# Performance work log

Measured on AMD Instinct MI355X. Metric: run time of the kernel, lower is better.

The kernel has to match this reference:

```python
import jax, jax.numpy as jnp
import numpy as np

N_NODES = 100000
N_EDGES = 3200000
N_GRAPHS = 512
F_IN, F_HID, F_OUT = 64, 16, 2


def gcn_conv(x, W, b, row, col, ew, n_nodes):
    # PyG GCNConv (normalize=True, add_self_loops=True, fill_value=1.0):
    # out = D^{-1/2} (A + I) D^{-1/2} X W + b, edge weights included.
    loop = jnp.arange(n_nodes, dtype=row.dtype)
    row_f = jnp.concatenate([row, loop])
    col_f = jnp.concatenate([col, loop])
    ew_f = jnp.concatenate([ew, jnp.ones((n_nodes,), dtype=ew.dtype)])
    deg = jax.ops.segment_sum(ew_f, col_f, num_segments=n_nodes)
    dinv = jnp.where(deg > 0, jax.lax.rsqrt(jnp.where(deg > 0, deg, 1.0)), 0.0)
    norm = dinv[row_f] * ew_f * dinv[col_f]          # [E+N]
    h = x @ W                                        # [N, F_out] dense GEMM first (cheaper gather)
    msg = norm[:, None] * h[row_f]                   # gather + scale
    out = jax.ops.segment_sum(msg, col_f, num_segments=n_nodes)  # scatter-add
    return out + b


def setup_inputs() -> dict:
    key = jax.random.key(0)
    ks = jax.random.split(key, 10)
    x = jax.random.normal(ks[0], (N_NODES, F_IN), dtype=jnp.float32)
    edge_index = jax.random.randint(ks[1], (2, N_EDGES), 0, N_NODES, dtype=jnp.int64)
    edge_weight = jax.random.uniform(ks[2], (N_EDGES,), dtype=jnp.float32)
    batch = jnp.sort(jax.random.randint(ks[3], (N_NODES,), 0, N_GRAPHS, dtype=jnp.int64))
    s1 = 1.0 / np.sqrt(F_IN)
    s2 = 1.0 / np.sqrt(F_HID)
    W1 = jax.random.uniform(ks[4], (F_IN, F_HID), minval=-s1, maxval=s1, dtype=jnp.float32)
    b1 = jnp.zeros((F_HID,), dtype=jnp.float32)
    W2 = jax.random.uniform(ks[5], (F_HID, F_HID), minval=-s2, maxval=s2, dtype=jnp.float32)
    b2 = jnp.zeros((F_HID,), dtype=jnp.float32)
    Wfc = jax.random.uniform(ks[6], (F_HID, F_OUT), minval=-s2, maxval=s2, dtype=jnp.float32)
    bfc = jax.random.uniform(ks[7], (F_OUT,), minval=-s2, maxval=s2, dtype=jnp.float32)
    return {"x": x, "edge_index": edge_index, "edge_weight": edge_weight, "batch": batch,
            "W1": W1, "b1": b1, "W2": W2, "b2": b2, "Wfc": Wfc, "bfc": bfc}


def reference(x, edge_index, edge_weight, batch, W1, b1, W2, b2, Wfc, bfc):
    row, col = edge_index[0], edge_index[1]
    n = x.shape[0]
    h = gcn_conv(x, W1, b1, row, col, edge_weight, n)
    h = jax.nn.relu(h)
    # dropout p=0.2 is identity in eval mode
    h = gcn_conv(h, W2, b2, row, col, edge_weight, n)
    h = jax.nn.relu(h)
    # global_mean_pool over graph ids
    sums = jax.ops.segment_sum(h, batch, num_segments=N_GRAPHS)
    counts = jax.ops.segment_sum(jnp.ones((n,), dtype=h.dtype), batch, num_segments=N_GRAPHS)
    pooled = sums / jnp.maximum(counts, 1.0)[:, None]
    logits = pooled @ Wfc + bfc
    return jax.nn.log_softmax(logits, axis=1)
```

## Files before the change

### kernel.cpp

```cpp
#include <hip/hip_runtime.h>


#define BSH   6
#define BN    64
#define NB    1563
#define BCAP  2432
#define BCAP2 2688
#define CHUNK 8192
#define DEQ   (1.0f / 511.0f)

__device__ __forceinline__ float bf2f(unsigned short u) {
    return __uint_as_float(((unsigned)u) << 16);
}
__device__ __forceinline__ unsigned short f2bf(float f) {
    unsigned b = __float_as_uint(f);
    return (unsigned short)((b + 0x7FFFu + ((b >> 16) & 1u)) >> 16);
}

__global__ void bin_kernel(const int* __restrict__ row, const int* __restrict__ col,
                           const float* __restrict__ ew, unsigned* __restrict__ gcur,
                           unsigned* __restrict__ recs, int E) {
    __shared__ unsigned lcnt[NB];
    __shared__ unsigned lbase[NB];
    int tid = threadIdx.x;
    int e0 = blockIdx.x * CHUNK;
    int e1 = e0 + CHUNK; if (e1 > E) e1 = E;
    for (int i = tid; i < NB; i += blockDim.x) lcnt[i] = 0;
    __syncthreads();
    for (int e = e0 + tid; e < e1; e += blockDim.x)
        atomicAdd(&lcnt[((unsigned)col[e]) >> BSH], 1u);
    __syncthreads();
    for (int i = tid; i < NB; i += blockDim.x) lbase[i] = atomicAdd(&gcur[i], lcnt[i]);
    __syncthreads();
    for (int i = tid; i < NB; i += blockDim.x) lcnt[i] = 0;
    __syncthreads();
    for (int e = e0 + tid; e < e1; e += blockDim.x) {
        unsigned c = (unsigned)col[e];
        unsigned b = c >> BSH;
        unsigned q = __float2uint_rn(ew[e] * 511.0f);
        unsigned r = atomicAdd(&lcnt[b], 1u);
        unsigned slot = lbase[b] + r;
        if (slot < BCAP)
            recs[(size_t)b * BCAP + slot] = ((c & (BN - 1u)) << 26)
                                          | ((unsigned)row[e] << 9) | q;
    }
}

__global__ void __launch_bounds__(256) csr_kernel(
        const unsigned* __restrict__ recs, const unsigned* __restrict__ gcur,
        float* __restrict__ dinv, unsigned* __restrict__ s_off,
        unsigned* __restrict__ ecnt, unsigned* __restrict__ epack, int N) {
    __shared__ unsigned combo[BN];
    __shared__ unsigned pre[BN];
    __shared__ unsigned cur[BN];
    __shared__ unsigned stot;
    __shared__ unsigned srt[BCAP2];
    int b = blockIdx.x, tid = threadIdx.x;
    if (tid < BN) { combo[tid] = 0; cur[tid] = 0; }
    for (int k = tid; k < BCAP2; k += 256) srt[k] = 0;
    __syncthreads();
    int n = (int)gcur[b]; if (n > BCAP) n = BCAP;
    const unsigned* rb = recs + (size_t)b * BCAP;
    for (int k = tid; k < n; k += 256) {
        unsigned r = rb[k];
        atomicAdd(&combo[r >> 26], (1u << 20) | (r & 511u));
    }
    __syncthreads();
    if (tid < 64) {
        unsigned cb  = combo[tid];
        unsigned cnt = cb >> 20;
        float    deg = (float)(cb & 0xFFFFFu) * DEQ;
        unsigned asz = (cnt + 3u) & ~3u;
        unsigned sc = asz;
#pragma unroll
        for (int d = 1; d < 64; d <<= 1) {
            unsigned t2 = __shfl_up(sc, d, 64);
            if (tid >= d) sc += t2;
        }
        unsigned base = sc - asz;
        pre[tid] = base;
        if (tid == 63) stot = sc;
        int i = (b << BSH) + tid;
        if (i < N) {
            dinv[i]  = rsqrtf(deg + 1.0f);
            s_off[i] = (unsigned)b * BCAP2 + base;
            ecnt[i]  = asz;
        }
    }
    __syncthreads();
    for (int k = tid; k < n; k += 256) {
        unsigned r = rb[k];
        unsigned o = r >> 26;
        unsigned p = pre[o] + atomicAdd(&cur[o], 1u);
        if (p < (unsigned)BCAP2) srt[p] = r & 0x03FFFFFFu;
    }
    __syncthreads();
    unsigned tot = stot; if (tot > (unsigned)BCAP2) tot = BCAP2;
    unsigned* eb = epack + (size_t)b * BCAP2;
    for (unsigned k = tid; k < tot; k += 256) eb[k] = srt[k];
}

__global__ void bounds_kernel(const int* __restrict__ batch, unsigned* __restrict__ gfirst,
                              unsigned* __restrict__ gend, int N) {
    int i = blockIdx.x * blockDim.x + threadIdx.x;
    if (i >= N) return;
    int g = batch[i];
    if (i == 0 || batch[i - 1] != g) gfirst[g] = (unsigned)i;
    if (i == N - 1 || batch[i + 1] != g) gend[g] = (unsigned)(i + 1);
}

__global__ void gemm1_kernel(const float* __restrict__ x, const float* __restrict__ W1,
                             const float* __restrict__ dinv, unsigned short* __restrict__ ys,
                             int N) {
    __shared__ float Ws[64 * 16];
    for (int k = threadIdx.x; k < 64 * 16; k += blockDim.x) Ws[k] = W1[k];
    __syncthreads();
    int i = blockIdx.x * blockDim.x + threadIdx.x;
    if (i >= N) return;
    const float4* xp = reinterpret_cast<const float4*>(x + (size_t)i * 64);
    float acc[16];
#pragma unroll
    for (int j = 0; j < 16; ++j) acc[j] = 0.0f;
#pragma unroll
    for (int k4 = 0; k4 < 16; ++k4) {
        float4 xv = xp[k4];
#pragma unroll
        for (int j = 0; j < 16; ++j) {
            acc[j] += xv.x * Ws[(k4 * 4 + 0) * 16 + j]
                    + xv.y * Ws[(k4 * 4 + 1) * 16 + j]
                    + xv.z * Ws[(k4 * 4 + 2) * 16 + j]
                    + xv.w * Ws[(k4 * 4 + 3) * 16 + j];
        }
    }
    float d = dinv[i];
    unsigned pk[8];
#pragma unroll
    for (int q = 0; q < 8; ++q)
        pk[q] = (unsigned)f2bf(d * acc[2 * q]) | ((unsigned)f2bf(d * acc[2 * q + 1]) << 16);
    uint4* op = reinterpret_cast<uint4*>(ys + (size_t)i * 16);
    op[0] = make_uint4(pk[0], pk[1], pk[2], pk[3]);
    op[1] = make_uint4(pk[4], pk[5], pk[6], pk[7]);
}

#define GREC(r, accq) { unsigned _r = (r); \
    accq += (float)(_r & 511u) * bf2f(ys[(size_t)(_r >> 9) * 16 + j]); }

__global__ void gconv1_kernel(const unsigned* __restrict__ s_off, const unsigned* __restrict__ ecnt,
                              const unsigned* __restrict__ epack, const float* __restrict__ dinv,
                              const unsigned short* __restrict__ ys,
                              const float* __restrict__ b1, const float* __restrict__ W2,
                              unsigned short* __restrict__ ys2, int N) {
    __shared__ float Ws[16 * 16];
    __shared__ float bs[16];
    if (threadIdx.x < 16 * 16) Ws[threadIdx.x] = W2[threadIdx.x];
    if (threadIdx.x < 16) bs[threadIdx.x] = b1[threadIdx.x];
    __syncthreads();
    int t = blockIdx.x * blockDim.x + threadIdx.x;
    int i = t >> 4, j = t & 15;
    if (i >= N) return;
    unsigned s = s_off[i], m = ecnt[i];
    const uint4* ep4 = reinterpret_cast<const uint4*>(epack + s);
    float accq = 0.0f;
    unsigned q4 = m >> 2, k = 0;
    for (; k + 2 <= q4; k += 2) {
        uint4 a = ep4[k], b4 = ep4[k + 1];
        GREC(a.x, accq); GREC(a.y, accq); GREC(a.z, accq); GREC(a.w, accq);
        GREC(b4.x, accq); GREC(b4.y, accq); GREC(b4.z, accq); GREC(b4.w, accq);
    }
    if (k < q4) {
        uint4 a = ep4[k];
        GREC(a.x, accq); GREC(a.y, accq); GREC(a.z, accq); GREC(a.w, accq);
    }
    float acc = bf2f(ys[(size_t)i * 16 + j]) + accq * DEQ;
    float d = dinv[i];
    float h = fmaxf(d * acc + bs[j], 0.0f);
    float acc2 = 0.0f;
#pragma unroll
    for (int kk = 0; kk < 16; ++kk) {
        float hk = __shfl(h, kk, 16);
        acc2 += hk * Ws[kk * 16 + j];
    }
    ys2[(size_t)i * 16 + j] = f2bf(d * acc2);
}

__global__ void gconv2_kernel(const unsigned* __restrict__ s_off, const unsigned* __restrict__ ecnt,
                              const unsigned* __restrict__ epack, const float* __restrict__ dinv,
                              const unsigned short* __restrict__ ys,
                              const float* __restrict__ bias, float* __restrict__ hbuf, int N) {
    int t = blockIdx.x * blockDim.x + threadIdx.x;
    int i = t >> 4, j = t & 15;
    if (i >= N) return;
    unsigned s = s_off[i], m = ecnt[i];
    const uint4* ep4 = reinterpret_cast<const uint4*>(epack + s);
    float accq = 0.0f;
    unsigned q4 = m >> 2, k = 0;
    for (; k + 2 <= q4; k += 2) {
        uint4 a = ep4[k], b4 = ep4[k + 1];
        GREC(a.x, accq); GREC(a.y, accq); GREC(a.z, accq); GREC(a.w, accq);
        GREC(b4.x, accq); GREC(b4.y, accq); GREC(b4.z, accq); GREC(b4.w, accq);
    }
    if (k < q4) {
        uint4 a = ep4[k];
        GREC(a.x, accq); GREC(a.y, accq); GREC(a.z, accq); GREC(a.w, accq);
    }
    float acc = bf2f(ys[(size_t)i * 16 + j]) + accq * DEQ;
    hbuf[(size_t)i * 16 + j] = fmaxf(dinv[i] * acc + bias[j], 0.0f);
}

__global__ void pool_kernel(const float* __restrict__ hbuf, const unsigned* __restrict__ gfirst,
                            const unsigned* __restrict__ gend, float* __restrict__ pooled, int G) {
    __shared__ float part[16][16];
    int g = blockIdx.x;
    unsigned s = gfirst[g], e = (s == 0xFFFFFFFFu) ? 0u : gend[g];
    int tid = threadIdx.x;
    int grp = tid >> 4, j = tid & 15;
    float acc = 0.0f;
    if (s != 0xFFFFFFFFu)
        for (unsigned i = s + grp; i < e; i += 16)
            acc += hbuf[(size_t)i * 16 + j];
    part[grp][j] = acc;
    __syncthreads();
    if (grp == 0) {
        float sum = 0.0f;
#pragma unroll
        for (int k = 0; k < 16; ++k) sum += part[k][j];
        float cnt = (s == 0xFFFFFFFFu) ? 1.0f : fmaxf((float)(e - s), 1.0f);
        pooled[g * 16 + j] = sum / cnt;
    }
}

__global__ void head_kernel(const float* __restrict__ pooled, const float* __restrict__ Wfc,
                            const float* __restrict__ bfc, float* __restrict__ out, int G) {
    int g = blockIdx.x * blockDim.x + threadIdx.x;
    if (g >= G) return;
    float l0 = bfc[0], l1 = bfc[1];
#pragma unroll
    for (int j = 0; j < 16; ++j) {
        float p = pooled[g * 16 + j];
        l0 += p * Wfc[j * 2 + 0];
        l1 += p * Wfc[j * 2 + 1];
    }
    float m = fmaxf(l0, l1);
    float lse = m + logf(expf(l0 - m) + expf(l1 - m));
    out[g * 2 + 0] = l0 - lse;
    out[g * 2 + 1] = l1 - lse;
}

__global__ void deg_at_kernel(const int* __restrict__ col, const float* __restrict__ ew,
                              float* __restrict__ deg, int E) {
    int t = blockIdx.x * blockDim.x + threadIdx.x;
    if (t < E) atomicAdd(&deg[col[t]], ew[t]);
}
__global__ void dinv_at_kernel(float* __restrict__ deg, const int* __restrict__ batch,
                               float* __restrict__ cntg, int N) {
    int i = blockIdx.x * blockDim.x + threadIdx.x;
    if (i >= N) return;
    deg[i] = rsqrtf(deg[i] + 1.0f);
    atomicAdd(&cntg[batch[i]], 1.0f);
}
__global__ void selfloop_kernel(const float* __restrict__ xw, const float* __restrict__ dinv,
                                float* __restrict__ out, int N) {
    int t = blockIdx.x * blockDim.x + threadIdx.x;
    if (t >= N * 16) return;
    float d = dinv[t >> 4];
    out[t] = d * d * xw[t];
}
__global__ void edge_at_kernel(const int* __restrict__ row, const int* __restrict__ col,
                               const float* __restrict__ ew, const float* __restrict__ dinv,
                               const float* __restrict__ xw, float* __restrict__ out, int E) {
    int t = blockIdx.x * blockDim.x + threadIdx.x;
    if (t >= E * 16) return;
    int e = t >> 4, j = t & 15;
    int r = row[e], c = col[e];
    float norm = dinv[r] * ew[e] * dinv[c];
    atomicAdd(&out[c * 16 + j], norm * xw[r * 16 + j]);
}
__global__ void pool_at_kernel(const float* __restrict__ h, const float* __restrict__ b2,
                               const int* __restrict__ batch, float* __restrict__ pooled, int N) {
    int t = blockIdx.x * blockDim.x + threadIdx.x;
    if (t >= N * 16) return;
    int i = t >> 4, j = t & 15;
    float v = fmaxf(h[t] + b2[j], 0.0f);
    atomicAdd(&pooled[batch[i] * 16 + j], v);
}
__global__ void head_at_kernel(const float* __restrict__ pooled, const float* __restrict__ cntg,
                               const float* __restrict__ Wfc, const float* __restrict__ bfc,
                               float* __restrict__ out, int G) {
    int g = blockIdx.x * blockDim.x + threadIdx.x;
    if (g >= G) return;
    float c = fmaxf(cntg[g], 1.0f);
    float l0 = bfc[0], l1 = bfc[1];
#pragma unroll
    for (int j = 0; j < 16; ++j) {
        float p = pooled[g * 16 + j] / c;
        l0 += p * Wfc[j * 2 + 0];
        l1 += p * Wfc[j * 2 + 1];
    }
    float m = fmaxf(l0, l1);
    float lse = m + logf(expf(l0 - m) + expf(l1 - m));
    out[g * 2 + 0] = l0 - lse;
    out[g * 2 + 1] = l1 - lse;
}
__global__ void gemm1p_kernel(const float* __restrict__ x, const float* __restrict__ W1,
                              float* __restrict__ xw, int N) {
    __shared__ float Ws[64 * 16];
    for (int k = threadIdx.x; k < 64 * 16; k += blockDim.x) Ws[k] = W1[k];
    __syncthreads();
    int i = blockIdx.x * blockDim.x + threadIdx.x;
    if (i >= N) return;
    const float4* xp = reinterpret_cast<const float4*>(x + (size_t)i * 64);
    float acc[16];
#pragma unroll
    for (int j = 0; j < 16; ++j) acc[j] = 0.0f;
#pragma unroll
    for (int k4 = 0; k4 < 16; ++k4) {
        float4 xv = xp[k4];
#pragma unroll
        for (int j = 0; j < 16; ++j) {
            acc[j] += xv.x * Ws[(k4 * 4 + 0) * 16 + j]
                    + xv.y * Ws[(k4 * 4 + 1) * 16 + j]
                    + xv.z * Ws[(k4 * 4 + 2) * 16 + j]
                    + xv.w * Ws[(k4 * 4 + 3) * 16 + j];
        }
    }
    float4* op = reinterpret_cast<float4*>(xw + (size_t)i * 16);
    op[0] = make_float4(acc[0],acc[1],acc[2],acc[3]);
    op[1] = make_float4(acc[4],acc[5],acc[6],acc[7]);
    op[2] = make_float4(acc[8],acc[9],acc[10],acc[11]);
    op[3] = make_float4(acc[12],acc[13],acc[14],acc[15]);
}
__global__ void gemm2p_kernel(const float* __restrict__ in, const float* __restrict__ b,
                              const float* __restrict__ W, float* __restrict__ xw, int N) {
    __shared__ float Ws[16 * 16];
    __shared__ float bs[16];
    if (threadIdx.x < 16 * 16) Ws[threadIdx.x] = W[threadIdx.x];
    if (threadIdx.x < 16) bs[threadIdx.x] = b[threadIdx.x];
    __syncthreads();
    int i = blockIdx.x * blockDim.x + threadIdx.x;
    if (i >= N) return;
    const float4* ip = reinterpret_cast<const float4*>(in + (size_t)i * 16);
    float h[16];
#pragma unroll
    for (int q = 0; q < 4; ++q) {
        float4 v = ip[q];
        h[q*4+0] = fmaxf(v.x + bs[q*4+0], 0.0f);
        h[q*4+1] = fmaxf(v.y + bs[q*4+1], 0.0f);
        h[q*4+2] = fmaxf(v.z + bs[q*4+2], 0.0f);
        h[q*4+3] = fmaxf(v.w + bs[q*4+3], 0.0f);
    }
    float acc[16];
#pragma unroll
    for (int j = 0; j < 16; ++j) acc[j] = 0.0f;
#pragma unroll
    for (int k = 0; k < 16; ++k)
#pragma unroll
        for (int j = 0; j < 16; ++j) acc[j] += h[k] * Ws[k * 16 + j];
    float4* op = reinterpret_cast<float4*>(xw + (size_t)i * 16);
    op[0] = make_float4(acc[0],acc[1],acc[2],acc[3]);
    op[1] = make_float4(acc[4],acc[5],acc[6],acc[7]);
    op[2] = make_float4(acc[8],acc[9],acc[10],acc[11]);
    op[3] = make_float4(acc[12],acc[13],acc[14],acc[15]);
}

extern "C" void kernel_launch(void* const* d_in, const int* in_sizes, int n_in,
                              void* d_out, int out_size, void* d_ws, size_t ws_size,
                              hipStream_t stream) {
    const float* x   = (const float*)d_in[0];
    const int*   ei  = (const int*)d_in[1];
    const float* ew  = (const float*)d_in[2];
    const int*   bat = (const int*)d_in[3];
    const float* W1  = (const float*)d_in[4];
    const float* b1  = (const float*)d_in[5];
    const float* W2  = (const float*)d_in[6];
    const float* b2  = (const float*)d_in[7];
    const float* Wfc = (const float*)d_in[8];
    const float* bfc = (const float*)d_in[9];
    float* out = (float*)d_out;

    const int N = in_sizes[0] / 64;
    const int E = in_sizes[2];
    const int G = out_size / 2;

    const int* row = ei;
    const int* col = ei + E;
    const size_t n16 = (size_t)N * 16;
    const int nb = (N + BN - 1) >> BSH;

    const size_t need = (size_t)NB * BCAP * 4
                      + (size_t)NB * BCAP2 * 4
                      + n16 * 2 * 2
                      + n16 * 4
                      + ((size_t)N * 3 + NB + (size_t)G * 18) * 4;

    const int B = 256;
    const int nbN   = (N + B - 1) / B;
    const int nbN16 = (int)((n16 + B - 1) / B);

    if (ws_size >= need && nb <= NB) {
        unsigned*       recs  = (unsigned*)d_ws;
        unsigned*       epack = recs + (size_t)NB * BCAP;
        unsigned short* ys    = (unsigned short*)(epack + (size_t)NB * BCAP2);
        unsigned short* ys2   = ys + n16;
        float*          hbuf  = (float*)(ys2 + n16);
        float*          dinv  = hbuf + n16;
        unsigned*       s_off = (unsigned*)(dinv + N);
        unsigned*       ecnt  = s_off + N;
        unsigned*       gcur  = ecnt + N;
        unsigned*       gfirst= gcur + NB;
        unsigned*       gend  = gfirst + G;
        float*          pooled= (float*)(gend + G);

        hipMemsetAsync(gcur, 0, (size_t)NB * 4, stream);
        hipMemsetAsync(gfirst, 0xFF, (size_t)G * 4, stream);
        hipMemsetAsync(gend, 0, (size_t)G * 4, stream);

        const int nbBin = (E + CHUNK - 1) / CHUNK;
        bin_kernel<<<nbBin, B, 0, stream>>>(row, col, ew, gcur, recs, E);
        csr_kernel<<<nb, B, 0, stream>>>(recs, gcur, dinv, s_off, ecnt, epack, N);
        bounds_kernel<<<nbN, B, 0, stream>>>(bat, gfirst, gend, N);

        gemm1_kernel<<<nbN, B, 0, stream>>>(x, W1, dinv, ys, N);
        gconv1_kernel<<<nbN16, B, 0, stream>>>(s_off, ecnt, epack, dinv, ys, b1, W2, ys2, N);
        gconv2_kernel<<<nbN16, B, 0, stream>>>(s_off, ecnt, epack, dinv, ys2, b2, hbuf, N);
        pool_kernel<<<G, B, 0, stream>>>(hbuf, gfirst, gend, pooled, G);
        head_kernel<<<(G + B - 1) / B, B, 0, stream>>>(pooled, Wfc, bfc, out, G);
    } else {
        float* xw1    = (float*)d_ws;
        float* out1   = xw1 + n16;
        float* dinv   = out1 + n16;
        float* pooled = dinv + N;
        float* cntg   = pooled + (size_t)G * 16;

        hipMemsetAsync(dinv, 0, (size_t)(N + G * 16 + G) * 4, stream);

        const int nbE   = (E + B - 1) / B;
        const int nbE16 = (int)(((long long)E * 16 + B - 1) / B);
        deg_at_kernel<<<nbE, B, 0, stream>>>(col, ew, dinv, E);
        dinv_at_kernel<<<nbN, B, 0, stream>>>(dinv, bat, cntg, N);
        gemm1p_kernel<<<nbN, B, 0, stream>>>(x, W1, xw1, N);
        selfloop_kernel<<<nbN16, B, 0, stream>>>(xw1, dinv, out1, N);
        edge_at_kernel<<<nbE16, B, 0, stream>>>(row, col, ew, dinv, xw1, out1, E);
        gemm2p_kernel<<<nbN, B, 0, stream>>>(out1, b1, W2, xw1, N);
        selfloop_kernel<<<nbN16, B, 0, stream>>>(xw1, dinv, out1, N);
        edge_at_kernel<<<nbE16, B, 0, stream>>>(row, col, ew, dinv, xw1, out1, E);
        pool_at_kernel<<<nbN16, B, 0, stream>>>(out1, b2, bat, pooled, N);
        head_at_kernel<<<(G + B - 1) / B, B, 0, stream>>>(pooled, cntg, Wfc, bfc, out, G);
    }
}
```

Before: 236.3 us.

## Partition edge-binning buffers per XCD to localize global atomics and writes

The bin kernel now reads the hardware XCC id and uses a separate counter array and record buffer for each of the 8 XCDs, so the global atomics on bin cursors and the scattered record writes stay within one XCD's L2. The CSR kernel then walks all 8 partitions per bin to build the degree sums and the sorted edge lists. The aim is to cut cross-die coherence traffic and atomic contention on the shared counters. In exchange it adds more workspace, 8 reads per bin in the CSR pass, and a per-partition capacity (RCAP) that could overflow if one XCD's share of a bin is skewed.

```diff
diff --git a/kernel.cpp b/kernel.cpp
--- a/kernel.cpp
+++ b/kernel.cpp
@@ -4,6 +4,8 @@
 #define BSH   6
 #define BN    64
 #define NB    1563
+#define NXCD  8
+#define RCAP  448
 #define BCAP  2432
 #define BCAP2 2688
 #define CHUNK 8192
@@ -16,13 +18,19 @@
     unsigned b = __float_as_uint(f);
     return (unsigned short)((b + 0x7FFFu + ((b >> 16) & 1u)) >> 16);
 }
+__device__ __forceinline__ int get_xcc() {
+    int x;
+    asm volatile("s_getreg_b32 %0, hwreg(HW_REG_XCC_ID)" : "=s"(x));
+    return x & (NXCD - 1);
+}
 
 __global__ void bin_kernel(const int* __restrict__ row, const int* __restrict__ col,
-                           const float* __restrict__ ew, unsigned* __restrict__ gcur,
-                           unsigned* __restrict__ recs, int E) {
+                           const float* __restrict__ ew, unsigned* __restrict__ gcur8,
+                           unsigned* __restrict__ recs8, int E) {
     __shared__ unsigned lcnt[NB];
     __shared__ unsigned lbase[NB];
     int tid = threadIdx.x;
+    int xcc = get_xcc();
     int e0 = blockIdx.x * CHUNK;
     int e1 = e0 + CHUNK; if (e1 > E) e1 = E;
     for (int i = tid; i < NB; i += blockDim.x) lcnt[i] = 0;
@@ -30,24 +38,26 @@
     for (int e = e0 + tid; e < e1; e += blockDim.x)
         atomicAdd(&lcnt[((unsigned)col[e]) >> BSH], 1u);
     __syncthreads();
-    for (int i = tid; i < NB; i += blockDim.x) lbase[i] = atomicAdd(&gcur[i], lcnt[i]);
+    unsigned* gc = gcur8 + (size_t)xcc * NB;
+    for (int i = tid; i < NB; i += blockDim.x) lbase[i] = atomicAdd(&gc[i], lcnt[i]);
     __syncthreads();
     for (int i = tid; i < NB; i += blockDim.x) lcnt[i] = 0;
     __syncthreads();
+    unsigned* rr = recs8 + (size_t)xcc * NB * RCAP;
     for (int e = e0 + tid; e < e1; e += blockDim.x) {
         unsigned c = (unsigned)col[e];
         unsigned b = c >> BSH;
         unsigned q = __float2uint_rn(ew[e] * 511.0f);
         unsigned r = atomicAdd(&lcnt[b], 1u);
         unsigned slot = lbase[b] + r;
-        if (slot < BCAP)
-            recs[(size_t)b * BCAP + slot] = ((c & (BN - 1u)) << 26)
-                                          | ((unsigned)row[e] << 9) | q;
+        if (slot < RCAP)
+            rr[(size_t)b * RCAP + slot] = ((c & (BN - 1u)) << 26)
+                                        | ((unsigned)row[e] << 9) | q;
     }
 }
 
 __global__ void __launch_bounds__(256) csr_kernel(
-        const unsigned* __restrict__ recs, const unsigned* __restrict__ gcur,
+        const unsigned* __restrict__ recs8, const unsigned* __restrict__ gcur8,
         float* __restrict__ dinv, unsigned* __restrict__ s_off,
         unsigned* __restrict__ ecnt, unsigned* __restrict__ epack, int N) {
     __shared__ unsigned combo[BN];
@@ -59,11 +69,13 @@
     if (tid < BN) { combo[tid] = 0; cur[tid] = 0; }
     for (int k = tid; k < BCAP2; k += 256) srt[k] = 0;
     __syncthreads();
-    int n = (int)gcur[b]; if (n > BCAP) n = BCAP;
-    const unsigned* rb = recs + (size_t)b * BCAP;
-    for (int k = tid; k < n; k += 256) {
-        unsigned r = rb[k];
-        atomicAdd(&combo[r >> 26], (1u << 20) | (r & 511u));
+    for (int x = 0; x < NXCD; ++x) {
+        int n = (int)gcur8[(size_t)x * NB + b]; if (n > RCAP) n = RCAP;
+        const unsigned* rb = recs8 + ((size_t)x * NB + b) * RCAP;
+        for (int k = tid; k < n; k += 256) {
+            unsigned r = rb[k];
+            atomicAdd(&combo[r >> 26], (1u << 20) | (r & 511u));
+        }
     }
     __syncthreads();
     if (tid < 64) {
@@ -88,11 +100,15 @@
         }
     }
     __syncthreads();
-    for (int k = tid; k < n; k += 256) {
-        unsigned r = rb[k];
-        unsigned o = r >> 26;
-        unsigned p = pre[o] + atomicAdd(&cur[o], 1u);
-        if (p < (unsigned)BCAP2) srt[p] = r & 0x03FFFFFFu;
+    for (int x = 0; x < NXCD; ++x) {
+        int n = (int)gcur8[(size_t)x * NB + b]; if (n > RCAP) n = RCAP;
+        const unsigned* rb = recs8 + ((size_t)x * NB + b) * RCAP;
+        for (int k = tid; k < n; k += 256) {
+            unsigned r = rb[k];
+            unsigned o = r >> 26;
+            unsigned p = pre[o] + atomicAdd(&cur[o], 1u);
+            if (p < (unsigned)BCAP2) srt[p] = r & 0x03FFFFFFu;
+        }
     }
     __syncthreads();
     unsigned tot = stot; if (tot > (unsigned)BCAP2) tot = BCAP2;
@@ -386,37 +402,37 @@
     const size_t n16 = (size_t)N * 16;
     const int nb = (N + BN - 1) >> BSH;
 
-    const size_t need = (size_t)NB * BCAP * 4
+    const size_t need = (size_t)NXCD * NB * RCAP * 4
                       + (size_t)NB * BCAP2 * 4
                       + n16 * 2 * 2
                       + n16 * 4
-                      + ((size_t)N * 3 + NB + (size_t)G * 18) * 4;
+                      + ((size_t)N * 3 + (size_t)NXCD * NB + (size_t)G * 18) * 4;
 
     const int B = 256;
     const int nbN   = (N + B - 1) / B;
     const int nbN16 = (int)((n16 + B - 1) / B);
 
     if (ws_size >= need && nb <= NB) {
-        unsigned*       recs  = (unsigned*)d_ws;
-        unsigned*       epack = recs + (size_t)NB * BCAP;
+        unsigned*       recs8 = (unsigned*)d_ws;
+        unsigned*       epack = recs8 + (size_t)NXCD * NB * RCAP;
         unsigned short* ys    = (unsigned short*)(epack + (size_t)NB * BCAP2);
         unsigned short* ys2   = ys + n16;
         float*          hbuf  = (float*)(ys2 + n16);
         float*          dinv  = hbuf + n16;
         unsigned*       s_off = (unsigned*)(dinv + N);
         unsigned*       ecnt  = s_off + N;
-        unsigned*       gcur  = ecnt + N;
-        unsigned*       gfirst= gcur + NB;
+        unsigned*       gcur8 = ecnt + N;
+        unsigned*       gfirst= gcur8 + (size_t)NXCD * NB;
         unsigned*       gend  = gfirst + G;
         float*          pooled= (float*)(gend + G);
 
-        hipMemsetAsync(gcur, 0, (size_t)NB * 4, stream);
+        hipMemsetAsync(gcur8, 0, (size_t)NXCD * NB * 4, stream);
         hipMemsetAsync(gfirst, 0xFF, (size_t)G * 4, stream);
         hipMemsetAsync(gend, 0, (size_t)G * 4, stream);
 
         const int nbBin = (E + CHUNK - 1) / CHUNK;
-        bin_kernel<<<nbBin, B, 0, stream>>>(row, col, ew, gcur, recs, E);
-        csr_kernel<<<nb, B, 0, stream>>>(recs, gcur, dinv, s_off, ecnt, epack, N);
+        bin_kernel<<<nbBin, B, 0, stream>>>(row, col, ew, gcur8, recs8, E);
+        csr_kernel<<<nb, B, 0, stream>>>(recs8, gcur8, dinv, s_off, ecnt, epack, N);
         bounds_kernel<<<nbN, B, 0, stream>>>(bat, gfirst, gend, N);
 
         gemm1_kernel<<<nbN, B, 0, stream>>>(x, W1, dinv, ys, N);
```

Measured after the change: 217.4 us. -8.0%, faster.
